# Performance work log

Measured on AMD Instinct MI355X. Metric: run time of the kernel, lower is better.

## Reference

```python
import jax, jax.numpy as jnp
import numpy as np

J, L = 4, 8
M = N = 128
B = 2
EPS = 1e-6  # abs_eps smoothing: |z|_eps = sqrt(re^2 + im^2 + eps)


def indices_third_order(J, L):
    # For each bandpass filter i = j1*L + l1, pair with every filter of scale
    # j2 >= j1 (all L angles) plus the lowpass (index J*L).
    # Count = J*L*(L*(J+1)/2 + 1) == num_coefficients.
    i_list, j_list = [], []
    for j1 in range(J):
        for l1 in range(L):
            i = j1 * L + l1
            for j2 in range(j1, J):
                for l2 in range(L):
                    i_list.append(i)
                    j_list.append(j2 * L + l2)
            i_list.append(i)
            j_list.append(J * L)
    return np.asarray(i_list), np.asarray(j_list)


def make_filters(J, L, M, N):
    # Real frequency-domain Morlet-like Gaussian bumps at J scales x L angles,
    # plus one lowpass. Shape (1, J*L+1, M, N), float32.
    kx = 2.0 * np.pi * np.fft.fftfreq(M)[:, None]
    ky = 2.0 * np.pi * np.fft.fftfreq(N)[None, :]
    filts = []
    for j in range(J):
        k0 = 0.8 * np.pi / 2.0 ** j
        sigma = 0.5 * k0
        for l in range(L):
            theta = np.pi * l / L
            cx, cy = k0 * np.cos(theta), k0 * np.sin(theta)
            filts.append(np.exp(-((kx - cx) ** 2 + (ky - cy) ** 2) / (2.0 * sigma ** 2)))
    sigma_lp = 0.8 * np.pi / 2.0 ** J
    filts.append(np.exp(-(kx ** 2 + ky ** 2) / (2.0 * sigma_lp ** 2)))
    return np.stack(filts)[None].astype(np.float32)


def abs_eps(z):
    return jnp.sqrt(z.real ** 2 + z.imag ** 2 + EPS)


def setup_inputs() -> dict:
    key = jax.random.key(0)
    x = jax.random.normal(key, (B, 1, M, N), dtype=jnp.float32)
    filters = jnp.asarray(make_filters(J, L, M, N))  # (1, 33, M, N)
    return {"x": x, "filters": filters}


def reference(x, filters):
    idx0, idx1 = indices_third_order(J, L)
    # first-order filtering: (B, nf, M, N) complex
    xf = jnp.fft.ifft2(filters * jnp.fft.fft2(x))
    xa = abs_eps(xf)  # real (B, nf, M, N)
    # cross-scale correlation: (B, nf_i, nf_j, M, N)
    inner = jnp.fft.ifft2(filters[:, None] * jnp.fft.fft2(xa)[:, :, None])
    out = jnp.real(jnp.conj(xf)[:, None] * inner).mean(axis=(-2, -1))  # (B, nf, nf)
    return out[:, idx0, idx1]  # (B, 672)
```

## Files before the change

### kernel.cpp

```cpp
#include <hip/hip_runtime.h>
#include <math.h>


#define PI_F 3.14159265358979323846f

__device__ __forceinline__ void make_tw(int lane, float* twr, float* twi) {
#pragma unroll
  for (int s = 0; s < 6; ++s) {
    int h = 32 >> s;
    float ang = -PI_F * (float)(lane & (h - 1)) / (float)h;
    float sv, cv;
    __sincosf(ang, &sv, &cv);
    twr[s] = cv; twi[s] = sv;
  }
  float ang = -PI_F * (float)lane / 64.0f;
  float sv, cv;
  __sincosf(ang, &sv, &cv);
  twr[6] = cv; twi[6] = sv;
}

template <int S>
__device__ __forceinline__ void fft128_dif(float& ar, float& ai, float& br, float& bi,
                                           const float* twr, const float* twi, int lane) {
  float s6r = twr[6], s6i = (S > 0) ? twi[6] : -twi[6];
  float ur = ar + br, ui = ai + bi;
  float vr = ar - br, vi = ai - bi;
  ar = ur; ai = ui;
  br = vr * s6r - vi * s6i;
  bi = vr * s6i + vi * s6r;
#pragma unroll
  for (int s = 0; s < 5; ++s) {
    int h = 32 >> s;
    float wr = twr[s], wi = (S > 0) ? twi[s] : -twi[s];
    bool hi = (lane & h) != 0;
    float pr, pi2;
    pr = __shfl_xor(ar, h, 64); pi2 = __shfl_xor(ai, h, 64);
    if (!hi) { ar += pr; ai += pi2; }
    else { float dr = pr - ar, di = pi2 - ai; ar = dr * wr - di * wi; ai = dr * wi + di * wr; }
    pr = __shfl_xor(br, h, 64); pi2 = __shfl_xor(bi, h, 64);
    if (!hi) { br += pr; bi += pi2; }
    else { float dr = pr - br, di = pi2 - bi; br = dr * wr - di * wi; bi = dr * wi + di * wr; }
  }
  {
    bool hi = (lane & 1) != 0;
    float pr, pi2;
    pr = __shfl_xor(ar, 1, 64); pi2 = __shfl_xor(ai, 1, 64);
    if (!hi) { ar += pr; ai += pi2; } else { ar = pr - ar; ai = pi2 - ai; }
    pr = __shfl_xor(br, 1, 64); pi2 = __shfl_xor(bi, 1, 64);
    if (!hi) { br += pr; bi += pi2; } else { br = pr - br; bi = pi2 - bi; }
  }
}

template <int NC>
__device__ __forceinline__ void transpose_r2c_n(float (&dr)[16], float (&di)[16],
    float (&er)[NC], float (&ei)[NC], float (&fr)[NC], float (&fi2)[NC],
    float2 (*tile)[128], int lane, int w, int colbase) {
#pragma unroll
  for (int ch = 0; ch < 2; ++ch) {
    if ((w >> 3) == ch) {
#pragma unroll
      for (int t = 0; t < 8; ++t) {
        int r = w * 8 + t;
        int rr = r & 63, sw = r & 15;
        tile[rr][lane ^ sw] = make_float2(dr[2 * t], di[2 * t]);
        tile[rr][(lane + 64) ^ sw] = make_float2(dr[2 * t + 1], di[2 * t + 1]);
      }
    }
    __syncthreads();
    {
      int sw = lane & 15;
#pragma unroll
      for (int ci = 0; ci < NC; ++ci) {
        int c = colbase + w * NC + ci;
        float2 v = tile[lane][c ^ sw];
        if (ch == 0) { er[ci] = v.x; ei[ci] = v.y; }
        else { fr[ci] = v.x; fi2[ci] = v.y; }
      }
    }
    __syncthreads();
  }
}

__device__ __forceinline__ void make_tw2(int q, float* t2r, float* t2i, float* hw) {
#pragma unroll
  for (int s = 0; s < 5; ++s) {
    int h = 16 >> s;
    float ang = -PI_F * (float)(q & (h - 1)) / (float)h;
    float sv, cv;
    __sincosf(ang, &sv, &cv);
    t2r[s] = cv; t2i[s] = sv;
  }
  float sv, cv;
  __sincosf(-PI_F * (float)q / 64.0f, &sv, &cv);         hw[0] = cv; hw[1] = sv;
  __sincosf(-PI_F * (float)(q + 32) / 64.0f, &sv, &cv);  hw[2] = cv; hw[3] = sv;
  __sincosf(-PI_F * (float)q / 32.0f, &sv, &cv);         hw[4] = cv; hw[5] = sv;
}

template <int S>
__device__ __forceinline__ void fft128x2_dif(float (&cr)[4], float (&ci)[4],
    const float* t2r, const float* t2i, const float* hw, int q) {
  float T0r = hw[0], T0i = (S > 0) ? hw[1] : -hw[1];
  float T1r = hw[2], T1i = (S > 0) ? hw[3] : -hw[3];
  float T2r = hw[4], T2i = (S > 0) ? hw[5] : -hw[5];
  {
    float ur = cr[0] + cr[2], ui = ci[0] + ci[2];
    float vr = cr[0] - cr[2], vi = ci[0] - ci[2];
    cr[0] = ur; ci[0] = ui;
    cr[2] = vr * T0r - vi * T0i; ci[2] = vr * T0i + vi * T0r;
    ur = cr[1] + cr[3]; ui = ci[1] + ci[3];
    vr = cr[1] - cr[3]; vi = ci[1] - ci[3];
    cr[1] = ur; ci[1] = ui;
    cr[3] = vr * T1r - vi * T1i; ci[3] = vr * T1i + vi * T1r;
  }
  {
    float ur = cr[0] + cr[1], ui = ci[0] + ci[1];
    float vr = cr[0] - cr[1], vi = ci[0] - ci[1];
    cr[0] = ur; ci[0] = ui;
    cr[1] = vr * T2r - vi * T2i; ci[1] = vr * T2i + vi * T2r;
    ur = cr[2] + cr[3]; ui = ci[2] + ci[3];
    vr = cr[2] - cr[3]; vi = ci[2] - ci[3];
    cr[2] = ur; ci[2] = ui;
    cr[3] = vr * T2r - vi * T2i; ci[3] = vr * T2i + vi * T2r;
  }
#pragma unroll
  for (int s = 0; s < 4; ++s) {
    int h = 16 >> s;
    float wr = t2r[s], wi = (S > 0) ? t2i[s] : -t2i[s];
    bool hi = (q & h) != 0;
#pragma unroll
    for (int m = 0; m < 4; ++m) {
      float pr = __shfl_xor(cr[m], h, 64);
      float pi2 = __shfl_xor(ci[m], h, 64);
      if (!hi) { cr[m] += pr; ci[m] += pi2; }
      else { float dr = pr - cr[m], di = pi2 - ci[m];
             cr[m] = dr * wr - di * wi; ci[m] = dr * wi + di * wr; }
    }
  }
  {
    bool hi = (q & 1) != 0;
#pragma unroll
    for (int m = 0; m < 4; ++m) {
      float pr = __shfl_xor(cr[m], 1, 64);
      float pi2 = __shfl_xor(ci[m], 1, 64);
      if (!hi) { cr[m] += pr; ci[m] += pi2; }
      else { cr[m] = pr - cr[m]; ci[m] = pi2 - ci[m]; }
    }
  }
}

__global__ __launch_bounds__(1024, 2) void k_prep(const float* __restrict__ x,
    float2* __restrict__ X, float* __restrict__ out, const float* __restrict__ F,
    float* __restrict__ G) {
  __shared__ float2 tile[64][128];
  int tid = threadIdx.x;
  int bx = blockIdx.x;
  if (bx == 8) {
    if (tid < 1344) out[tid] = 0.f;
    return;
  }
  if (bx >= 9) {
    int q = bx - 9;
    int j = q >> 2, part = q & 3;
    const float* Fj = F + j * 16384;
    float* Gj = G + j * 16384;
#pragma unroll
    for (int it = 0; it < 4; ++it) {
      int k = part * 4096 + it * 1024 + tid;
      int u = k >> 7, v = k & 127;
      int un = (128 - u) & 127, vn = (128 - v) & 127;
      float f = Fj[k], fn = Fj[un * 128 + vn];
      Gj[k] = 0.5f * (f * f + fn * fn);
    }
    return;
  }
  int b = bx >> 2, quarter = bx & 3;
  int lane = tid & 63, w = tid >> 6;
  float twr[7], twi[7]; make_tw(lane, twr, twi);
  const float* xb = x + b * 16384;
  int u0 = __brev((unsigned)lane) >> 25;
  int spA = __brev((unsigned)((128 - u0) & 127)) >> 25;
  int spB = __brev((unsigned)(127 - u0)) >> 25;
  float dr[16], di[16];
  float er[2], ei[2], fr[2], fi2[2];
#pragma unroll
  for (int t = 0; t < 4; ++t) {
    int r0 = w * 8 + 2 * t;
    float ar = xb[r0 * 128 + lane],      ai2 = xb[(r0 + 1) * 128 + lane];
    float br = xb[r0 * 128 + lane + 64], bi  = xb[(r0 + 1) * 128 + lane + 64];
    fft128_dif<1>(ar, ai2, br, bi, twr, twi, lane);
    int la = spA & 63;
    float fAr = __shfl(ar, la, 64), fAi = __shfl(ai2, la, 64);
    float fBr = __shfl(br, la, 64), fBi = __shfl(bi, la, 64);
    float Pr = (spA < 64) ? fAr : fBr, Pi = (spA < 64) ? fAi : fBi;
    float X0r = 0.5f * (ar + Pr),  X0i = 0.5f * (ai2 - Pi);
    float X1r = 0.5f * (ai2 + Pi), X1i = 0.5f * (Pr - ar);
    int lb = spB & 63;
    float gAr = __shfl(ar, lb, 64), gAi = __shfl(ai2, lb, 64);
    float gBr = __shfl(br, lb, 64), gBi = __shfl(bi, lb, 64);
    float Qr = (spB < 64) ? gAr : gBr, Qi = (spB < 64) ? gAi : gBi;
    float Y0r = 0.5f * (br + Qr), Y0i = 0.5f * (bi - Qi);
    float Y1r = 0.5f * (bi + Qi), Y1i = 0.5f * (Qr - br);
    dr[2 * (2 * t)] = X0r;     di[2 * (2 * t)] = X0i;
    dr[2 * (2 * t) + 1] = Y0r; di[2 * (2 * t) + 1] = Y0i;
    dr[2 * (2 * t + 1)] = X1r;     di[2 * (2 * t + 1)] = X1i;
    dr[2 * (2 * t + 1) + 1] = Y1r; di[2 * (2 * t + 1) + 1] = Y1i;
  }
  transpose_r2c_n<2>(dr, di, er, ei, fr, fi2, tile, lane, w, quarter * 32);
#pragma unroll
  for (int ci = 0; ci < 2; ++ci) {
    int c = quarter * 32 + w * 2 + ci;
    float ar = er[ci], ai2 = ei[ci], br = fr[ci], bi = fi2[ci];
    fft128_dif<1>(ar, ai2, br, bi, twr, twi, lane);
    int vn = __brev((unsigned)c) >> 25;
    X[b * 16384 + u0 * 128 + vn] = make_float2(ar, ai2);
    X[b * 16384 + (u0 + 1) * 128 + vn] = make_float2(br, bi);
  }
}

__global__ __launch_bounds__(1024, 1) void k_fields(const float2* __restrict__ X,
    const float* __restrict__ F, const float* __restrict__ G,
    float* __restrict__ dfld, float* __restrict__ xa) {
  __shared__ float2 tile[64][128];
  int tid = threadIdx.x, lane = tid & 63, w = tid >> 6;
  int g = lane >> 5, q = lane & 31;
  int bx = blockIdx.x;
  bool isd = (bx < 68);
  int b, half;
  bool has1 = false;
  const float* g0 = nullptr; const float* g1 = nullptr; const float* Fb = nullptr;
  float* o0; float* o1 = nullptr;
  if (isd) {
    int dp = bx >> 1; half = bx & 1;
    b = dp / 17; int p = dp - b * 17;
    int j0 = 2 * p; has1 = (p < 16);
    g0 = G + j0 * 16384;
    g1 = G + (j0 + 1) * 16384;
    o0 = dfld + (b * 33 + j0) * 16384;
    o1 = dfld + (b * 33 + j0 + 1) * 16384;
  } else {
    int qq = bx - 68; int qi = qq >> 1; half = qq & 1;
    b = qi >> 5; int f = qi & 31;
    Fb = F + f * 16384;
    o0 = xa + qi * 16384;
  }
  float t2r[5], t2i[5], hw[6];
  make_tw2(q, t2r, t2i, hw);
  const float2* Xb = X + b * 16384;

  float sr[4][4], si[4][4];
#pragma unroll
  for (int k = 0; k < 4; ++k) {
    int r = w * 8 + 2 * k + g;
    float cr[4], ci[4];
#pragma unroll
    for (int m = 0; m < 4; ++m) {
      int p = q + 32 * m;
      float2 xv = Xb[r * 128 + p];
      if (isd) {
        float ga = g0[r * 128 + p];
        float gb = has1 ? g1[r * 128 + p] : 0.f;
        cr[m] = xv.x * ga - xv.y * gb; ci[m] = xv.y * ga + xv.x * gb;
      } else {
        float f0 = Fb[r * 128 + p];
        cr[m] = xv.x * f0; ci[m] = xv.y * f0;
      }
    }
    fft128x2_dif<-1>(cr, ci, t2r, t2i, hw, q);
#pragma unroll
    for (int m = 0; m < 4; ++m) { sr[k][m] = cr[m]; si[k][m] = ci[m]; }
  }

  float pr[2][4], pi2a[2][4];
  int colbase = half * 64;
#pragma unroll
  for (int ch = 0; ch < 2; ++ch) {
    if ((w >> 3) == ch) {
#pragma unroll
      for (int k = 0; k < 4; ++k) {
        int r = w * 8 + 2 * k + g;
        int rr = r & 63, sw = r & 15;
#pragma unroll
        for (int m = 0; m < 4; ++m)
          tile[rr][(32 * m + q) ^ sw] = make_float2(sr[k][m], si[k][m]);
      }
    }
    __syncthreads();
    {
      int sw = q & 15;
#pragma unroll
      for (int j = 0; j < 2; ++j) {
        int c = colbase + w * 4 + 2 * j + g;
#pragma unroll
        for (int mm = 0; mm < 2; ++mm) {
          float2 v = tile[32 * mm + q][c ^ sw];
          pr[j][2 * ch + mm] = v.x; pi2a[j][2 * ch + mm] = v.y;
        }
      }
    }
    __syncthreads();
  }

  const float sc = 1.0f / 16384.0f;
#pragma unroll
  for (int j = 0; j < 2; ++j) {
    fft128x2_dif<-1>(pr[j], pi2a[j], t2r, t2i, hw, q);
    int c = colbase + w * 4 + 2 * j + g;
#pragma unroll
    for (int m = 0; m < 4; ++m) {
      int su = 32 * m + q;
      if (isd) {
        o0[c * 128 + su] = pr[j][m];
        if (has1) o1[c * 128 + su] = pi2a[j][m];
      } else {
        float tr = pr[j][m] * sc, ti = pi2a[j][m] * sc;
        o0[c * 128 + su] = sqrtf(tr * tr + ti * ti + 1e-6f);
      }
    }
  }
}

__global__ __launch_bounds__(512) void k_dot(const float* __restrict__ xa,
    const float* __restrict__ dfld, float* __restrict__ out) {
  int qb = blockIdx.x;
  int im = qb >> 4;
  int slice = (qb >> 2) & 3;
  int jq = qb & 3;
  int b = im >> 5, i = im & 31;
  int j0 = jq * 9;
  int t = threadIdx.x;
  const float4* xr = (const float4*)(xa + im * 16384 + slice * 4096);
  const float4* db = (const float4*)(dfld + (b * 33 + j0) * 16384 + slice * 4096);
  float acc[9];
#pragma unroll
  for (int j = 0; j < 9; ++j) acc[j] = 0.f;
#pragma unroll
  for (int it = 0; it < 2; ++it) {
    int k = it * 512 + t;
    float4 xv = xr[k];
#pragma unroll
    for (int j = 0; j < 9; ++j) {
      float4 dv = db[j * 4096 + k];
      acc[j] += xv.x * dv.x + xv.y * dv.y + xv.z * dv.z + xv.w * dv.w;
    }
  }
#pragma unroll
  for (int j = 0; j < 9; ++j) {
#pragma unroll
    for (int off = 32; off > 0; off >>= 1) acc[j] += __shfl_xor(acc[j], off, 64);
  }
  __shared__ float red[8][9];
  int w = t >> 6, lane = t & 63;
  if (lane == 0) {
#pragma unroll
    for (int j = 0; j < 9; ++j) red[w][j] = acc[j];
  }
  __syncthreads();
  if (t < 9) {
    int j = j0 + t;
    float s = 0.f;
#pragma unroll
    for (int w2 = 0; w2 < 8; ++w2) s += red[w2][t];
    int j1 = i >> 3, l1 = i & 7;
    const int pref[4] = {0, 264, 464, 600};
    int per = (4 - j1) * 8 + 1;
    int start = pref[j1] + l1 * per;
    int pos = -1;
    if (j == 32) pos = start + per - 1;
    else if (j < 32) {
      int j2 = j >> 3;
      if (j2 >= j1) pos = start + (j2 - j1) * 8 + (j & 7);
    }
    if (pos >= 0)
      atomicAdd(out + b * 672 + pos, s * (1.0f / 16384.0f) * (1.0f / 16384.0f));
  }
}

extern "C" void kernel_launch(void* const* d_in, const int* in_sizes, int n_in,
                              void* d_out, int out_size, void* d_ws, size_t ws_size,
                              hipStream_t stream) {
  (void)in_sizes; (void)n_in; (void)out_size; (void)ws_size;
  const float* x = (const float*)d_in[0];
  const float* F = (const float*)d_in[1];
  float* out = (float*)d_out;
  char* ws = (char*)d_ws;
  float2* X = (float2*)(ws + 0);
  float* dfld = (float*)(ws + 262144);
  float* xa = (float*)(ws + 4587520);
  float* G = (float*)(ws + 8781824);

  hipLaunchKernelGGL(k_prep, dim3(141), dim3(1024), 0, stream, x, X, out, F, G);
  hipLaunchKernelGGL(k_fields, dim3(196), dim3(1024), 0, stream, X, F, G, dfld, xa);
  hipLaunchKernelGGL(k_dot, dim3(1024), dim3(512), 0, stream, xa, dfld, out);
}
```

Before: 96.73 us.

## Use radix-4 style trivial twiddles in FFT stages and split prep into eighths

The second-to-last butterfly stage in both FFT routines now uses the trivial twiddles 1 and -i through swaps and negations instead of a complex multiply. Fewer twiddles are precomputed with sincos. The first two stages of the 4-element per-lane FFT are merged into a radix-4 butterfly. k_prep splits each batch's column pass into eighths rather than quarters, so there are more blocks with less work each. These changes cut ALU and register pressure, at the cost of a little extra row-FFT redundancy in k_prep.

Measured after the change: 95.88 us. No clear change (-0.9%).

```diff
diff --git a/kernel.cpp b/kernel.cpp
--- a/kernel.cpp
+++ b/kernel.cpp
@@ -6,7 +6,7 @@
 
 __device__ __forceinline__ void make_tw(int lane, float* twr, float* twi) {
 #pragma unroll
-  for (int s = 0; s < 6; ++s) {
+  for (int s = 0; s < 4; ++s) {
     int h = 32 >> s;
     float ang = -PI_F * (float)(lane & (h - 1)) / (float)h;
     float sv, cv;
@@ -16,20 +16,20 @@
   float ang = -PI_F * (float)lane / 64.0f;
   float sv, cv;
   __sincosf(ang, &sv, &cv);
-  twr[6] = cv; twi[6] = sv;
+  twr[4] = cv; twi[4] = sv;
 }
 
 template <int S>
 __device__ __forceinline__ void fft128_dif(float& ar, float& ai, float& br, float& bi,
                                            const float* twr, const float* twi, int lane) {
-  float s6r = twr[6], s6i = (S > 0) ? twi[6] : -twi[6];
+  float s6r = twr[4], s6i = (S > 0) ? twi[4] : -twi[4];
   float ur = ar + br, ui = ai + bi;
   float vr = ar - br, vi = ai - bi;
   ar = ur; ai = ui;
   br = vr * s6r - vi * s6i;
   bi = vr * s6i + vi * s6r;
 #pragma unroll
-  for (int s = 0; s < 5; ++s) {
+  for (int s = 0; s < 4; ++s) {
     int h = 32 >> s;
     float wr = twr[s], wi = (S > 0) ? twi[s] : -twi[s];
     bool hi = (lane & h) != 0;
@@ -42,6 +42,26 @@
     else { float dr = pr - br, di = pi2 - bi; br = dr * wr - di * wi; bi = dr * wi + di * wr; }
   }
   {
+    bool hi = (lane & 2) != 0, odd = (lane & 1) != 0;
+    float pr, pi2;
+    pr = __shfl_xor(ar, 2, 64); pi2 = __shfl_xor(ai, 2, 64);
+    if (!hi) { ar += pr; ai += pi2; }
+    else {
+      float dr = pr - ar, di = pi2 - ai;
+      if (!odd) { ar = dr; ai = di; }
+      else if (S > 0) { ar = di; ai = -dr; }
+      else { ar = -di; ai = dr; }
+    }
+    pr = __shfl_xor(br, 2, 64); pi2 = __shfl_xor(bi, 2, 64);
+    if (!hi) { br += pr; bi += pi2; }
+    else {
+      float dr = pr - br, di = pi2 - bi;
+      if (!odd) { br = dr; bi = di; }
+      else if (S > 0) { br = di; bi = -dr; }
+      else { br = -di; bi = dr; }
+    }
+  }
+  {
     bool hi = (lane & 1) != 0;
     float pr, pi2;
     pr = __shfl_xor(ar, 1, 64); pi2 = __shfl_xor(ai, 1, 64);
@@ -83,7 +103,7 @@
 
 __device__ __forceinline__ void make_tw2(int q, float* t2r, float* t2i, float* hw) {
 #pragma unroll
-  for (int s = 0; s < 5; ++s) {
+  for (int s = 0; s < 3; ++s) {
     int h = 16 >> s;
     float ang = -PI_F * (float)(q & (h - 1)) / (float)h;
     float sv, cv;
@@ -91,39 +111,33 @@
     t2r[s] = cv; t2i[s] = sv;
   }
   float sv, cv;
-  __sincosf(-PI_F * (float)q / 64.0f, &sv, &cv);         hw[0] = cv; hw[1] = sv;
-  __sincosf(-PI_F * (float)(q + 32) / 64.0f, &sv, &cv);  hw[2] = cv; hw[3] = sv;
-  __sincosf(-PI_F * (float)q / 32.0f, &sv, &cv);         hw[4] = cv; hw[5] = sv;
+  __sincosf(-PI_F * (float)q / 64.0f, &sv, &cv);        hw[0] = cv; hw[1] = sv;
+  __sincosf(-PI_F * (float)q / 32.0f, &sv, &cv);        hw[2] = cv; hw[3] = sv;
+  __sincosf(-3.0f * PI_F * (float)q / 64.0f, &sv, &cv); hw[4] = cv; hw[5] = sv;
 }
 
 template <int S>
 __device__ __forceinline__ void fft128x2_dif(float (&cr)[4], float (&ci)[4],
     const float* t2r, const float* t2i, const float* hw, int q) {
   float T0r = hw[0], T0i = (S > 0) ? hw[1] : -hw[1];
-  float T1r = hw[2], T1i = (S > 0) ? hw[3] : -hw[3];
-  float T2r = hw[4], T2i = (S > 0) ? hw[5] : -hw[5];
-  {
-    float ur = cr[0] + cr[2], ui = ci[0] + ci[2];
-    float vr = cr[0] - cr[2], vi = ci[0] - ci[2];
-    cr[0] = ur; ci[0] = ui;
-    cr[2] = vr * T0r - vi * T0i; ci[2] = vr * T0i + vi * T0r;
-    ur = cr[1] + cr[3]; ui = ci[1] + ci[3];
-    vr = cr[1] - cr[3]; vi = ci[1] - ci[3];
-    cr[1] = ur; ci[1] = ui;
-    cr[3] = vr * T1r - vi * T1i; ci[3] = vr * T1i + vi * T1r;
-  }
-  {
-    float ur = cr[0] + cr[1], ui = ci[0] + ci[1];
-    float vr = cr[0] - cr[1], vi = ci[0] - ci[1];
-    cr[0] = ur; ci[0] = ui;
-    cr[1] = vr * T2r - vi * T2i; ci[1] = vr * T2i + vi * T2r;
-    ur = cr[2] + cr[3]; ui = ci[2] + ci[3];
-    vr = cr[2] - cr[3]; vi = ci[2] - ci[3];
-    cr[2] = ur; ci[2] = ui;
-    cr[3] = vr * T2r - vi * T2i; ci[3] = vr * T2i + vi * T2r;
-  }
-#pragma unroll
-  for (int s = 0; s < 4; ++s) {
+  float T2r = hw[2], T2i = (S > 0) ? hw[3] : -hw[3];
+  float T3r = hw[4], T3i = (S > 0) ? hw[5] : -hw[5];
+  {
+    float t0r = cr[0] + cr[2], t0i = ci[0] + ci[2];
+    float t1r = cr[0] - cr[2], t1i = ci[0] - ci[2];
+    float s2r = cr[1] + cr[3], s2i = ci[1] + ci[3];
+    float t3r = cr[1] - cr[3], t3i = ci[1] - ci[3];
+    cr[0] = t0r + s2r; ci[0] = t0i + s2i;
+    float u1r = t0r - s2r, u1i = t0i - s2i;
+    cr[1] = u1r * T2r - u1i * T2i; ci[1] = u1r * T2i + u1i * T2r;
+    float v2r, v2i, v3r, v3i;
+    if (S > 0) { v2r = t1r + t3i; v2i = t1i - t3r; v3r = t1r - t3i; v3i = t1i + t3r; }
+    else       { v2r = t1r - t3i; v2i = t1i + t3r; v3r = t1r + t3i; v3i = t1i - t3r; }
+    cr[2] = v2r * T0r - v2i * T0i; ci[2] = v2r * T0i + v2i * T0r;
+    cr[3] = v3r * T3r - v3i * T3i; ci[3] = v3r * T3i + v3i * T3r;
+  }
+#pragma unroll
+  for (int s = 0; s < 3; ++s) {
     int h = 16 >> s;
     float wr = t2r[s], wi = (S > 0) ? t2i[s] : -t2i[s];
     bool hi = (q & h) != 0;
@@ -137,6 +151,21 @@
     }
   }
   {
+    bool hi = (q & 2) != 0, odd = (q & 1) != 0;
+#pragma unroll
+    for (int m = 0; m < 4; ++m) {
+      float pr = __shfl_xor(cr[m], 2, 64);
+      float pi2 = __shfl_xor(ci[m], 2, 64);
+      if (!hi) { cr[m] += pr; ci[m] += pi2; }
+      else {
+        float dr = pr - cr[m], di = pi2 - ci[m];
+        if (!odd) { cr[m] = dr; ci[m] = di; }
+        else if (S > 0) { cr[m] = di; ci[m] = -dr; }
+        else { cr[m] = -di; ci[m] = dr; }
+      }
+    }
+  }
+  {
     bool hi = (q & 1) != 0;
 #pragma unroll
     for (int m = 0; m < 4; ++m) {
@@ -154,12 +183,12 @@
   __shared__ float2 tile[64][128];
   int tid = threadIdx.x;
   int bx = blockIdx.x;
-  if (bx == 8) {
+  if (bx == 16) {
     if (tid < 1344) out[tid] = 0.f;
     return;
   }
-  if (bx >= 9) {
-    int q = bx - 9;
+  if (bx >= 17) {
+    int q = bx - 17;
     int j = q >> 2, part = q & 3;
     const float* Fj = F + j * 16384;
     float* Gj = G + j * 16384;
@@ -173,15 +202,15 @@
     }
     return;
   }
-  int b = bx >> 2, quarter = bx & 3;
+  int b = bx >> 3, eighth = bx & 7;
   int lane = tid & 63, w = tid >> 6;
-  float twr[7], twi[7]; make_tw(lane, twr, twi);
+  float twr[5], twi[5]; make_tw(lane, twr, twi);
   const float* xb = x + b * 16384;
   int u0 = __brev((unsigned)lane) >> 25;
   int spA = __brev((unsigned)((128 - u0) & 127)) >> 25;
   int spB = __brev((unsigned)(127 - u0)) >> 25;
   float dr[16], di[16];
-  float er[2], ei[2], fr[2], fi2[2];
+  float er[1], ei[1], fr[1], fi2[1];
 #pragma unroll
   for (int t = 0; t < 4; ++t) {
     int r0 = w * 8 + 2 * t;
@@ -205,11 +234,10 @@
     dr[2 * (2 * t + 1)] = X1r;     di[2 * (2 * t + 1)] = X1i;
     dr[2 * (2 * t + 1) + 1] = Y1r; di[2 * (2 * t + 1) + 1] = Y1i;
   }
-  transpose_r2c_n<2>(dr, di, er, ei, fr, fi2, tile, lane, w, quarter * 32);
-#pragma unroll
-  for (int ci = 0; ci < 2; ++ci) {
-    int c = quarter * 32 + w * 2 + ci;
-    float ar = er[ci], ai2 = ei[ci], br = fr[ci], bi = fi2[ci];
+  transpose_r2c_n<1>(dr, di, er, ei, fr, fi2, tile, lane, w, eighth * 16);
+  {
+    int c = eighth * 16 + w;
+    float ar = er[0], ai2 = ei[0], br = fr[0], bi = fi2[0];
     fft128_dif<1>(ar, ai2, br, bi, twr, twi, lane);
     int vn = __brev((unsigned)c) >> 25;
     X[b * 16384 + u0 * 128 + vn] = make_float2(ar, ai2);
@@ -243,7 +271,7 @@
     Fb = F + f * 16384;
     o0 = xa + qi * 16384;
   }
-  float t2r[5], t2i[5], hw[6];
+  float t2r[3], t2i[3], hw[6];
   make_tw2(q, t2r, t2i, hw);
   const float2* Xb = X + b * 16384;
 
@@ -388,7 +416,7 @@
   float* xa = (float*)(ws + 4587520);
   float* G = (float*)(ws + 8781824);
 
-  hipLaunchKernelGGL(k_prep, dim3(141), dim3(1024), 0, stream, x, X, out, F, G);
+  hipLaunchKernelGGL(k_prep, dim3(149), dim3(1024), 0, stream, x, X, out, F, G);
   hipLaunchKernelGGL(k_fields, dim3(196), dim3(1024), 0, stream, X, F, G, dfld, xa);
   hipLaunchKernelGGL(k_dot, dim3(1024), dim3(512), 0, stream, xa, dfld, out);
 }
```
